# Optimization experiments

Hardware: AMD Instinct MI355X
Metric: run time of the kernel (lower is better)

Reference implementation:

```python
import jax, jax.numpy as jnp
import numpy as np

EPS = 216.0 / 24389.0
KAPPA = 24389.0 / 27.0
WP = jnp.array([0.95047, 1.0, 1.08883], dtype=jnp.float32)  # D65 white point
M_RGB2XYZ = jnp.array([[0.4124564, 0.3575761, 0.1804375],
                       [0.2126729, 0.7151522, 0.0721750],
                       [0.0193339, 0.1191920, 0.9503041]], dtype=jnp.float32)
M_XYZ2RGB = jnp.array([[3.2404542, -1.5371385, -0.4985314],
                       [-0.9692660, 1.8760108, 0.0415560],
                       [0.0556434, -0.2040259, 1.0572252]], dtype=jnp.float32)
GRID = 8          # cv2.createCLAHE tileGridSize=(8,8)
CLIP_LIMIT = 2.0  # cv2.createCLAHE clipLimit=2.0
NBINS = 256


def _srgb_to_linear(c):
    return jnp.where(c <= 0.04045, c / 12.92, ((c + 0.055) / 1.055) ** 2.4)


def _linear_to_srgb(c):
    c = jnp.maximum(c, 0.0)
    return jnp.where(c <= 0.0031308, c * 12.92, 1.055 * c ** (1.0 / 2.4) - 0.055)


def _rgb_to_lab(rgb):  # rgb [...,3] in [0,1]
    xyz = _srgb_to_linear(rgb) @ M_RGB2XYZ.T / WP
    f = jnp.where(xyz > EPS, jnp.cbrt(xyz), (KAPPA * xyz + 16.0) / 116.0)
    L = 116.0 * f[..., 1] - 16.0
    a = 500.0 * (f[..., 0] - f[..., 1])
    b = 200.0 * (f[..., 1] - f[..., 2])
    return L, a, b


def _lab_to_rgb(L, a, b):
    fy = (L + 16.0) / 116.0
    fx = fy + a / 500.0
    fz = fy - b / 200.0
    def finv(f):
        f3 = f ** 3
        return jnp.where(f3 > EPS, f3, (116.0 * f - 16.0) / KAPPA)
    xyz = jnp.stack([finv(fx), finv(fy), finv(fz)], axis=-1) * WP
    return jnp.clip(_linear_to_srgb(xyz @ M_XYZ2RGB.T), 0.0, 1.0)


def _quantize_L(L):  # cv2.normalize(..., 0, 255, NORM_MINMAX) per image + uint8 cast
    lmin = L.min(axis=(1, 2), keepdims=True)
    lmax = L.max(axis=(1, 2), keepdims=True)
    l255 = (L - lmin) / (lmax - lmin + 1e-6) * 255.0
    return jnp.clip(jnp.round(l255), 0, 255).astype(jnp.int32)


def _equalize_hist(l_int):  # cv2.equalizeHist per image, [N,H,W] int32 -> float levels
    N, H, W = l_int.shape
    seg = (jnp.arange(N, dtype=jnp.int32)[:, None, None] * NBINS + l_int).reshape(-1)
    hist = jax.ops.segment_sum(jnp.ones(seg.shape, jnp.float32), seg,
                               num_segments=N * NBINS).reshape(N, NBINS)
    lut = jnp.round(jnp.cumsum(hist, axis=1) * (255.0 / (H * W)))  # [N,256]
    return jnp.take_along_axis(lut, l_int.reshape(N, H * W), axis=1).reshape(N, H, W)


def _clahe(l_int):  # tiled clipped histogram equalization + bilinear LUT blend
    N, H, W = l_int.shape
    th, tw = H // GRID, W // GRID
    area = th * tw
    ty = jnp.arange(H, dtype=jnp.int32) // th
    tx = jnp.arange(W, dtype=jnp.int32) // tw
    tile = ty[:, None] * GRID + tx[None, :]                      # [H,W] tile id
    seg = ((jnp.arange(N, dtype=jnp.int32)[:, None, None] * (GRID * GRID) + tile)
           * NBINS + l_int).reshape(-1)
    hist = jax.ops.segment_sum(jnp.ones(seg.shape, jnp.float32), seg,
                               num_segments=N * GRID * GRID * NBINS
                               ).reshape(N, GRID, GRID, NBINS)
    limit = max(CLIP_LIMIT * area / NBINS, 1.0)                  # = 32 for 64x64 tiles
    clipped = jnp.minimum(hist, limit)
    excess = (hist - clipped).sum(axis=-1, keepdims=True)
    luts = jnp.round(jnp.cumsum(clipped + excess / NBINS, axis=-1) * (255.0 / area))
    # bilinear interpolation between the 4 neighbouring tile LUTs (border-clamped)
    cy = jnp.clip((jnp.arange(H, dtype=jnp.float32) + 0.5) / th - 0.5, 0.0, GRID - 1.0)
    cx = jnp.clip((jnp.arange(W, dtype=jnp.float32) + 0.5) / tw - 0.5, 0.0, GRID - 1.0)
    y0 = jnp.clip(jnp.floor(cy).astype(jnp.int32), 0, GRID - 2); y1 = y0 + 1
    x0 = jnp.clip(jnp.floor(cx).astype(jnp.int32), 0, GRID - 2); x1 = x0 + 1
    wy = (cy - y0)[:, None]
    wx = (cx - x0)[None, :]
    def per_image(lut, v):  # lut [GRID,GRID,256], v [H,W]
        v00 = lut[y0[:, None], x0[None, :], v]
        v01 = lut[y0[:, None], x1[None, :], v]
        v10 = lut[y1[:, None], x0[None, :], v]
        v11 = lut[y1[:, None], x1[None, :], v]
        top = v00 * (1.0 - wx) + v01 * wx
        bot = v10 * (1.0 - wx) + v11 * wx
        return top * (1.0 - wy) + bot * wy
    return jax.vmap(per_image)(luts, l_int)


def setup_inputs() -> dict:
    key = jax.random.key(0)
    x = jax.random.uniform(key, (16, 3, 512, 512), dtype=jnp.float32)
    return {"x": x}


def reference(x):
    rgb = jnp.transpose(x, (0, 2, 3, 1))          # NCHW -> NHWC
    L, a, b = _rgb_to_lab(rgb)
    l_int = _quantize_L(L)
    def recon(l255):
        out = _lab_to_rgb(l255 * (100.0 / 255.0), a, b)
        return jnp.transpose(out, (0, 3, 1, 2)) * 255.0  # uint8-valued like original
    return recon(_equalize_hist(l_int)), recon(_clahe(l_int))
```

## Files before the change

### kernel.cpp

```cpp
#include <hip/hip_runtime.h>

#define NIMG 16
#define HH 512
#define WW 512
#define HW (HH * WW)
#define NHW (NIMG * HW)
#define TILE 64
#define TILE_AREA (TILE * TILE)

#define EPSV ((float)(216.0 / 24389.0))
#define KAPV ((float)(24389.0 / 27.0))


__device__ __forceinline__ float pow24(float t) {
    float l   = __builtin_amdgcn_logf(t);
    float r   = __builtin_amdgcn_exp2f(l);
    float dl  = (t - r) * __builtin_amdgcn_rcpf(r) * 1.4426950408889634f;
    float ehi = 2.4f * l;
    float elo = __builtin_fmaf(2.4f, l, -ehi) + 2.4f * dl;
    float p   = __builtin_amdgcn_exp2f(ehi);
    return __builtin_fmaf(p * 0.6931471805599453f, elo, p);
}

__device__ __forceinline__ float cbrt_p(float v) {
    float l  = __builtin_amdgcn_logf(v);
    float t  = __builtin_amdgcn_exp2f(l * (1.0f / 3.0f));
    float t2 = t * t;
    float num = __builtin_fmaf(-t2, t, v);
    return __builtin_fmaf(num, __builtin_amdgcn_rcpf(3.0f * t2), t);
}

__device__ __forceinline__ float srgb2lin_p(float c) {
    float lin = c / 12.92f;
    float t   = (c + 0.055f) / 1.055f;
    return (c <= 0.04045f) ? lin : pow24(t);
}

__device__ __forceinline__ float fwd_p(float v) {
    return (v > EPSV) ? cbrt_p(v) : (KAPV * v + 16.0f) / 116.0f;
}

__device__ __forceinline__ float lin2srgb_f(float c) {
    c = fmaxf(c, 0.0f);
    float lo = c * 12.92f;
    float p  = __builtin_amdgcn_exp2f(__builtin_amdgcn_logf(c) * (float)(1.0 / 2.4));
    float hi = 1.055f * p - 0.055f;
    float r  = (c <= 0.0031308f) ? lo : hi;
    return fminf(fmaxf(r, 0.0f), 1.0f);
}

__device__ __forceinline__ float finv_f(float f) {
    float f3 = f * f * f;
    return (f3 > EPSV) ? f3 : (116.0f * f - 16.0f) * (float)(27.0 / 24389.0);
}

__device__ __forceinline__ void lab2rgb255_f(float L, float a, float b,
                                             float* R, float* G, float* B) {
    float fy = (L + 16.0f) * (float)(1.0 / 116.0);
    float fx = fy + a * (float)(1.0 / 500.0);
    float fz = fy - b * (float)(1.0 / 200.0);
    float X = finv_f(fx) * 0.95047f;
    float Y = finv_f(fy);
    float Z = finv_f(fz) * 1.08883f;
    *R = lin2srgb_f((float)3.2404542 * X + (float)-1.5371385 * Y + (float)-0.4985314 * Z) * 255.0f;
    *G = lin2srgb_f((float)-0.969266 * X + (float)1.8760108  * Y + (float)0.041556   * Z) * 255.0f;
    *B = lin2srgb_f((float)0.0556434 * X + (float)-0.2040259 * Y + (float)1.0572252  * Z) * 255.0f;
}

__device__ __forceinline__ unsigned f2o(float f) {
    unsigned b = __float_as_uint(f);
    return (b & 0x80000000u) ? ~b : (b | 0x80000000u);
}
__device__ __forceinline__ float o2f(unsigned o) {
    return __uint_as_float((o & 0x80000000u) ? (o ^ 0x80000000u) : ~o);
}


__global__ void k_init(unsigned* mm) {
    int t = blockIdx.x * 256 + threadIdx.x;
    if (t < NIMG * 64)
        mm[t] = ((t & 63) < 32) ? 0xFFFFFFFFu : 0u;
}

__global__ void k_lab(const float* __restrict__ x, float* __restrict__ Lbuf,
                      unsigned* __restrict__ mm) {
    int n = blockIdx.y;
    const float* img = x + (size_t)n * 3 * HW;
    float* Lp = Lbuf + (size_t)n * HW;
    int base = blockIdx.x * 2048;
    float mn = 1e30f, mx = -1e30f;
    for (int i = 0; i < 2; i++) {
        int p = base + i * 1024 + threadIdx.x * 4;
        float4 r4 = *(const float4*)(img + p);
        float4 g4 = *(const float4*)(img + HW + p);
        float4 b4 = *(const float4*)(img + 2 * HW + p);
        float4 L4;
        #pragma unroll
        for (int k = 0; k < 4; k++) {
            float rr = ((const float*)&r4)[k];
            float gg = ((const float*)&g4)[k];
            float bb = ((const float*)&b4)[k];
            float rl = srgb2lin_p(rr), gl = srgb2lin_p(gg), bl = srgb2lin_p(bb);
            float Y = ((float)0.2126729 * rl + (float)0.7151522 * gl + (float)0.072175  * bl);
            float L = 116.0f * fwd_p(Y) - 16.0f;
            ((float*)&L4)[k] = L;
            mn = fminf(mn, L);
            mx = fmaxf(mx, L);
        }
        *(float4*)(Lp + p) = L4;
    }
    for (int off = 32; off; off >>= 1) {
        mn = fminf(mn, __shfl_down(mn, off, 64));
        mx = fmaxf(mx, __shfl_down(mx, off, 64));
    }
    __shared__ float smn[4], smx[4];
    int wv = threadIdx.x >> 6, ln = threadIdx.x & 63;
    if (ln == 0) { smn[wv] = mn; smx[wv] = mx; }
    __syncthreads();
    if (threadIdx.x == 0) {
        mn = fminf(fminf(smn[0], smn[1]), fminf(smn[2], smn[3]));
        mx = fmaxf(fmaxf(smx[0], smx[1]), fmaxf(smx[2], smx[3]));
        atomicMin(&mm[n * 64], f2o(mn));
        atomicMax(&mm[n * 64 + 32], f2o(mx));
    }
}

__global__ void k_quant_hist(const float* __restrict__ Lbuf, const unsigned* __restrict__ mm,
                             unsigned char* __restrict__ li_arr, int* __restrict__ hist_tile,
                             float* __restrict__ lut_tile) {
    int n = blockIdx.y, tile = blockIdx.x;
    int ty = tile >> 3, tx = tile & 7;
    int t = threadIdx.x;
    __shared__ int sh[256];
    sh[t] = 0;
    __syncthreads();
    float lmin = o2f(mm[n * 64]), lmax = o2f(mm[n * 64 + 32]);
    float d = lmax - lmin + (float)1e-6;
    const float* Lp = Lbuf + (size_t)n * HW;
    unsigned char* lio = li_arr + (size_t)n * HW;
    for (int i = t; i < TILE_AREA; i += 256) {
        int r = i >> 6, c = i & 63;
        int p = (ty * TILE + r) * WW + tx * TILE + c;
        float l255 = (Lp[p] - lmin) / d * 255.0f;
        int li = (int)rintf(l255);
        li = min(max(li, 0), 255);
        lio[p] = (unsigned char)li;
        atomicAdd(&sh[li], 1);
    }
    __syncthreads();
    int h = sh[t];
    hist_tile[(n * 64 + tile) * 256 + t] = h;

    int cl = min(h, 32);
    int sum = cl;
    for (int off = 32; off; off >>= 1) sum += __shfl_down(sum, off, 64);
    __shared__ int wsum[4];
    if ((t & 63) == 0) wsum[t >> 6] = sum;
    __syncthreads();
    int total = wsum[0] + wsum[1] + wsum[2] + wsum[3];
    int exc = TILE_AREA - total;
    sh[t] = 256 * cl + exc;
    __syncthreads();
    for (int off = 1; off < 256; off <<= 1) {
        int v = sh[t];
        int add = (t >= off) ? sh[t - off] : 0;
        __syncthreads();
        sh[t] = v + add;
        __syncthreads();
    }
    lut_tile[(n * 64 + tile) * 256 + t] =
        rintf((float)sh[t] * (float)(255.0 / 1048576.0));
}

__global__ void k_eq_lut(const int* __restrict__ hist_tile, float* __restrict__ lut_eq) {
    int n = blockIdx.x, t = threadIdx.x;
    const int* ht = hist_tile + n * 64 * 256;
    int h = 0;
    for (int tile = 0; tile < 64; tile++) h += ht[tile * 256 + t];
    __shared__ int s[256];
    s[t] = h;
    __syncthreads();
    for (int off = 1; off < 256; off <<= 1) {
        int v = s[t];
        int add = (t >= off) ? s[t - off] : 0;
        __syncthreads();
        s[t] = v + add;
        __syncthreads();
    }
    lut_eq[n * 256 + t] = rintf((float)s[t] * (float)(255.0 / (double)HW));
}

__global__ void k_recon(const float* __restrict__ x, const unsigned char* __restrict__ li_arr,
                        const float* __restrict__ lut_eq, const float* __restrict__ lut_tile,
                        float* __restrict__ out) {
    int n = blockIdx.y, tile = blockIdx.x;
    int ty = tile >> 3, tx = tile & 7;
    int t = threadIdx.x;
    __shared__ float slut[9 * 256];
    __shared__ float seq[256];
    seq[t] = lut_eq[n * 256 + t];
    const float* lt = lut_tile + n * 64 * 256;
    for (int j = t; j < 9 * 256; j += 256) {
        int q = j >> 8;
        int jy = q / 3, jx = q % 3;
        int gy = min(max(ty - 1 + jy, 0), 7);
        int gx = min(max(tx - 1 + jx, 0), 7);
        slut[j] = lt[(gy * 8 + gx) * 256 + (j & 255)];
    }
    __syncthreads();

    const float* img = x + (size_t)n * 3 * HW;
    const unsigned char* lip = li_arr + (size_t)n * HW;
    float* o0 = out + (size_t)n * 3 * HW;
    float* o1 = out + (size_t)3 * NHW + (size_t)n * 3 * HW;

    for (int it = 0; it < 4; it++) {
        int j = it * 1024 + t * 4;
        int r = j >> 6, c = j & 63;
        int y = ty * TILE + r;
        int xb = tx * TILE + c;
        int p = y * WW + xb;

        float4 r4 = *(const float4*)(img + p);
        float4 g4 = *(const float4*)(img + HW + p);
        float4 b4 = *(const float4*)(img + 2 * HW + p);
        uchar4 li4 = *(const uchar4*)(lip + p);

        float cyf = fminf(fmaxf(((float)y + 0.5f) / 64.0f - 0.5f, 0.0f), 7.0f);
        int y0 = min((int)cyf, 6);
        float wy = cyf - (float)y0;
        int ly = y0 - ty + 1;

        float4 R0, G0, B0, R1, G1, B1;
        #pragma unroll
        for (int k = 0; k < 4; k++) {
            float rr = ((const float*)&r4)[k];
            float gg = ((const float*)&g4)[k];
            float bb = ((const float*)&b4)[k];
            float rl = srgb2lin_p(rr), gl = srgb2lin_p(gg), bl = srgb2lin_p(bb);
            float X = ((float)0.4124564 * rl + (float)0.3575761 * gl + (float)0.1804375 * bl) / (float)0.95047;
            float Y = ((float)0.2126729 * rl + (float)0.7151522 * gl + (float)0.072175  * bl);
            float Z = ((float)0.0193339 * rl + (float)0.119192  * gl + (float)0.9503041 * bl) / (float)1.08883;
            float fx = fwd_p(X), fy = fwd_p(Y), fz = fwd_p(Z);
            float A  = 500.0f * (fx - fy);
            float B2 = 200.0f * (fy - fz);

            int li = ((const unsigned char*)&li4)[k];
            float l_eq = seq[li];

            int xc = xb + k;
            float cxf = fminf(fmaxf(((float)xc + 0.5f) / 64.0f - 0.5f, 0.0f), 7.0f);
            int x0 = min((int)cxf, 6);
            float wx = cxf - (float)x0;
            int lx = x0 - tx + 1;
            int base = ((ly * 3 + lx) << 8) + li;
            float v00 = slut[base];
            float v01 = slut[base + 256];
            float v10 = slut[base + 768];
            float v11 = slut[base + 1024];
            float top = v00 * (1.0f - wx) + v01 * wx;
            float bot = v10 * (1.0f - wx) + v11 * wx;
            float l_cl = top * (1.0f - wy) + bot * wy;

            float R, G, B;
            lab2rgb255_f(l_eq * (float)(100.0 / 255.0), A, B2, &R, &G, &B);
            ((float*)&R0)[k] = R; ((float*)&G0)[k] = G; ((float*)&B0)[k] = B;
            lab2rgb255_f(l_cl * (float)(100.0 / 255.0), A, B2, &R, &G, &B);
            ((float*)&R1)[k] = R; ((float*)&G1)[k] = G; ((float*)&B1)[k] = B;
        }
        *(float4*)(o0 + p)          = R0;
        *(float4*)(o0 + HW + p)     = G0;
        *(float4*)(o0 + 2 * HW + p) = B0;
        *(float4*)(o1 + p)          = R1;
        *(float4*)(o1 + HW + p)     = G1;
        *(float4*)(o1 + 2 * HW + p) = B1;
    }
}

extern "C" void kernel_launch(void* const* d_in, const int* in_sizes, int n_in,
                              void* d_out, int out_size, void* d_ws, size_t ws_size,
                              hipStream_t stream) {
    const float* x = (const float*)d_in[0];
    float* out = (float*)d_out;
    char* ws = (char*)d_ws;

    float* Lbuf = (float*)ws;
    size_t off = (size_t)NHW * 4;
    unsigned char* li = (unsigned char*)(ws + off); off += NHW;
    int* hist_tile = (int*)(ws + off);    off += NIMG * 64 * 256 * 4;
    float* lut_eq = (float*)(ws + off);   off += NIMG * 256 * 4;
    float* lut_tile = (float*)(ws + off); off += NIMG * 64 * 256 * 4;
    unsigned* mm = (unsigned*)(ws + off); off += NIMG * 64 * 4;

    k_init<<<4, 256, 0, stream>>>(mm);
    k_lab<<<dim3(HW / 2048, NIMG), 256, 0, stream>>>(x, Lbuf, mm);
    k_quant_hist<<<dim3(64, NIMG), 256, 0, stream>>>(Lbuf, mm, li, hist_tile, lut_tile);
    k_eq_lut<<<NIMG, 256, 0, stream>>>(hist_tile, lut_eq);
    k_recon<<<dim3(64, NIMG), 256, 0, stream>>>(x, li, lut_eq, lut_tile, out);
}
```

Before: 185.7 us.

## Compute full Lab once, stash a/b in output buffer, merge kernels into three

The first kernel now computes the full Lab conversion per 64x64 tile and writes the a and b channels into the first output's G/B planes as scratch. The reconstruction kernel reads them back instead of reloading RGB and recomputing the forward transform. The global atomic min/max and init kernel are replaced by per-tile partials that the quant kernel reduces, and the equalization LUT scan is folded into the reconstruction kernel. This avoids recomputing the transcendental-heavy forward path and cuts two launches. In exchange it adds extra writes and reads of a/b, redundant histogram summation in every reconstruction block, and in-place reuse of the output buffer.

```diff
diff --git a/kernel.cpp b/kernel.cpp
--- a/kernel.cpp
+++ b/kernel.cpp
@@ -67,171 +67,27 @@
     *B = lin2srgb_f((float)0.0556434 * X + (float)-0.2040259 * Y + (float)1.0572252  * Z) * 255.0f;
 }
 
-__device__ __forceinline__ unsigned f2o(float f) {
-    unsigned b = __float_as_uint(f);
-    return (b & 0x80000000u) ? ~b : (b | 0x80000000u);
-}
-__device__ __forceinline__ float o2f(unsigned o) {
-    return __uint_as_float((o & 0x80000000u) ? (o ^ 0x80000000u) : ~o);
-}
-
-
-__global__ void k_init(unsigned* mm) {
-    int t = blockIdx.x * 256 + threadIdx.x;
-    if (t < NIMG * 64)
-        mm[t] = ((t & 63) < 32) ? 0xFFFFFFFFu : 0u;
-}
-
-__global__ void k_lab(const float* __restrict__ x, float* __restrict__ Lbuf,
-                      unsigned* __restrict__ mm) {
-    int n = blockIdx.y;
+__global__ void k1_lab(const float* __restrict__ x, float* __restrict__ Lbuf,
+                       float* __restrict__ out, float* __restrict__ tmn,
+                       float* __restrict__ tmx) {
+    int n = blockIdx.y, tile = blockIdx.x;
+    int b = (n << 6) + tile;
+    int ty = tile >> 3, tx = tile & 7;
+    int t = threadIdx.x;
     const float* img = x + (size_t)n * 3 * HW;
     float* Lp = Lbuf + (size_t)n * HW;
-    int base = blockIdx.x * 2048;
+    float* o0 = out + (size_t)n * 3 * HW;
+
     float mn = 1e30f, mx = -1e30f;
-    for (int i = 0; i < 2; i++) {
-        int p = base + i * 1024 + threadIdx.x * 4;
+    #pragma unroll
+    for (int it = 0; it < 4; it++) {
+        int j = it * 1024 + t * 4;
+        int r = j >> 6, c = j & 63;
+        int p = (ty * TILE + r) * WW + tx * TILE + c;
         float4 r4 = *(const float4*)(img + p);
         float4 g4 = *(const float4*)(img + HW + p);
         float4 b4 = *(const float4*)(img + 2 * HW + p);
-        float4 L4;
-        #pragma unroll
-        for (int k = 0; k < 4; k++) {
-            float rr = ((const float*)&r4)[k];
-            float gg = ((const float*)&g4)[k];
-            float bb = ((const float*)&b4)[k];
-            float rl = srgb2lin_p(rr), gl = srgb2lin_p(gg), bl = srgb2lin_p(bb);
-            float Y = ((float)0.2126729 * rl + (float)0.7151522 * gl + (float)0.072175  * bl);
-            float L = 116.0f * fwd_p(Y) - 16.0f;
-            ((float*)&L4)[k] = L;
-            mn = fminf(mn, L);
-            mx = fmaxf(mx, L);
-        }
-        *(float4*)(Lp + p) = L4;
-    }
-    for (int off = 32; off; off >>= 1) {
-        mn = fminf(mn, __shfl_down(mn, off, 64));
-        mx = fmaxf(mx, __shfl_down(mx, off, 64));
-    }
-    __shared__ float smn[4], smx[4];
-    int wv = threadIdx.x >> 6, ln = threadIdx.x & 63;
-    if (ln == 0) { smn[wv] = mn; smx[wv] = mx; }
-    __syncthreads();
-    if (threadIdx.x == 0) {
-        mn = fminf(fminf(smn[0], smn[1]), fminf(smn[2], smn[3]));
-        mx = fmaxf(fmaxf(smx[0], smx[1]), fmaxf(smx[2], smx[3]));
-        atomicMin(&mm[n * 64], f2o(mn));
-        atomicMax(&mm[n * 64 + 32], f2o(mx));
-    }
-}
-
-__global__ void k_quant_hist(const float* __restrict__ Lbuf, const unsigned* __restrict__ mm,
-                             unsigned char* __restrict__ li_arr, int* __restrict__ hist_tile,
-                             float* __restrict__ lut_tile) {
-    int n = blockIdx.y, tile = blockIdx.x;
-    int ty = tile >> 3, tx = tile & 7;
-    int t = threadIdx.x;
-    __shared__ int sh[256];
-    sh[t] = 0;
-    __syncthreads();
-    float lmin = o2f(mm[n * 64]), lmax = o2f(mm[n * 64 + 32]);
-    float d = lmax - lmin + (float)1e-6;
-    const float* Lp = Lbuf + (size_t)n * HW;
-    unsigned char* lio = li_arr + (size_t)n * HW;
-    for (int i = t; i < TILE_AREA; i += 256) {
-        int r = i >> 6, c = i & 63;
-        int p = (ty * TILE + r) * WW + tx * TILE + c;
-        float l255 = (Lp[p] - lmin) / d * 255.0f;
-        int li = (int)rintf(l255);
-        li = min(max(li, 0), 255);
-        lio[p] = (unsigned char)li;
-        atomicAdd(&sh[li], 1);
-    }
-    __syncthreads();
-    int h = sh[t];
-    hist_tile[(n * 64 + tile) * 256 + t] = h;
-
-    int cl = min(h, 32);
-    int sum = cl;
-    for (int off = 32; off; off >>= 1) sum += __shfl_down(sum, off, 64);
-    __shared__ int wsum[4];
-    if ((t & 63) == 0) wsum[t >> 6] = sum;
-    __syncthreads();
-    int total = wsum[0] + wsum[1] + wsum[2] + wsum[3];
-    int exc = TILE_AREA - total;
-    sh[t] = 256 * cl + exc;
-    __syncthreads();
-    for (int off = 1; off < 256; off <<= 1) {
-        int v = sh[t];
-        int add = (t >= off) ? sh[t - off] : 0;
-        __syncthreads();
-        sh[t] = v + add;
-        __syncthreads();
-    }
-    lut_tile[(n * 64 + tile) * 256 + t] =
-        rintf((float)sh[t] * (float)(255.0 / 1048576.0));
-}
-
-__global__ void k_eq_lut(const int* __restrict__ hist_tile, float* __restrict__ lut_eq) {
-    int n = blockIdx.x, t = threadIdx.x;
-    const int* ht = hist_tile + n * 64 * 256;
-    int h = 0;
-    for (int tile = 0; tile < 64; tile++) h += ht[tile * 256 + t];
-    __shared__ int s[256];
-    s[t] = h;
-    __syncthreads();
-    for (int off = 1; off < 256; off <<= 1) {
-        int v = s[t];
-        int add = (t >= off) ? s[t - off] : 0;
-        __syncthreads();
-        s[t] = v + add;
-        __syncthreads();
-    }
-    lut_eq[n * 256 + t] = rintf((float)s[t] * (float)(255.0 / (double)HW));
-}
-
-__global__ void k_recon(const float* __restrict__ x, const unsigned char* __restrict__ li_arr,
-                        const float* __restrict__ lut_eq, const float* __restrict__ lut_tile,
-                        float* __restrict__ out) {
-    int n = blockIdx.y, tile = blockIdx.x;
-    int ty = tile >> 3, tx = tile & 7;
-    int t = threadIdx.x;
-    __shared__ float slut[9 * 256];
-    __shared__ float seq[256];
-    seq[t] = lut_eq[n * 256 + t];
-    const float* lt = lut_tile + n * 64 * 256;
-    for (int j = t; j < 9 * 256; j += 256) {
-        int q = j >> 8;
-        int jy = q / 3, jx = q % 3;
-        int gy = min(max(ty - 1 + jy, 0), 7);
-        int gx = min(max(tx - 1 + jx, 0), 7);
-        slut[j] = lt[(gy * 8 + gx) * 256 + (j & 255)];
-    }
-    __syncthreads();
-
-    const float* img = x + (size_t)n * 3 * HW;
-    const unsigned char* lip = li_arr + (size_t)n * HW;
-    float* o0 = out + (size_t)n * 3 * HW;
-    float* o1 = out + (size_t)3 * NHW + (size_t)n * 3 * HW;
-
-    for (int it = 0; it < 4; it++) {
-        int j = it * 1024 + t * 4;
-        int r = j >> 6, c = j & 63;
-        int y = ty * TILE + r;
-        int xb = tx * TILE + c;
-        int p = y * WW + xb;
-
-        float4 r4 = *(const float4*)(img + p);
-        float4 g4 = *(const float4*)(img + HW + p);
-        float4 b4 = *(const float4*)(img + 2 * HW + p);
-        uchar4 li4 = *(const uchar4*)(lip + p);
-
-        float cyf = fminf(fmaxf(((float)y + 0.5f) / 64.0f - 0.5f, 0.0f), 7.0f);
-        int y0 = min((int)cyf, 6);
-        float wy = cyf - (float)y0;
-        int ly = y0 - ty + 1;
-
-        float4 R0, G0, B0, R1, G1, B1;
+        float4 L4, A4, B4;
         #pragma unroll
         for (int k = 0; k < 4; k++) {
             float rr = ((const float*)&r4)[k];
@@ -242,10 +98,163 @@
             float Y = ((float)0.2126729 * rl + (float)0.7151522 * gl + (float)0.072175  * bl);
             float Z = ((float)0.0193339 * rl + (float)0.119192  * gl + (float)0.9503041 * bl) / (float)1.08883;
             float fx = fwd_p(X), fy = fwd_p(Y), fz = fwd_p(Z);
-            float A  = 500.0f * (fx - fy);
-            float B2 = 200.0f * (fy - fz);
-
+            float L = 116.0f * fy - 16.0f;
+            ((float*)&L4)[k] = L;
+            ((float*)&A4)[k] = 500.0f * (fx - fy);
+            ((float*)&B4)[k] = 200.0f * (fy - fz);
+            mn = fminf(mn, L);
+            mx = fmaxf(mx, L);
+        }
+        *(float4*)(Lp + p)          = L4;
+        *(float4*)(o0 + HW + p)     = A4;
+        *(float4*)(o0 + 2 * HW + p) = B4;
+    }
+    for (int off = 32; off; off >>= 1) {
+        mn = fminf(mn, __shfl_down(mn, off, 64));
+        mx = fmaxf(mx, __shfl_down(mx, off, 64));
+    }
+    __shared__ float smn[4], smx[4];
+    int wv = t >> 6, ln = t & 63;
+    if (ln == 0) { smn[wv] = mn; smx[wv] = mx; }
+    __syncthreads();
+    if (t == 0) {
+        tmn[b] = fminf(fminf(smn[0], smn[1]), fminf(smn[2], smn[3]));
+        tmx[b] = fmaxf(fmaxf(smx[0], smx[1]), fmaxf(smx[2], smx[3]));
+    }
+}
+
+__global__ void k2_quant(const float* __restrict__ Lbuf, const float* __restrict__ tmn,
+                         const float* __restrict__ tmx, unsigned char* __restrict__ li_arr,
+                         int* __restrict__ hist_tile, float* __restrict__ lut_tile) {
+    int n = blockIdx.y, tile = blockIdx.x;
+    int b = (n << 6) + tile;
+    int ty = tile >> 3, tx = tile & 7;
+    int t = threadIdx.x;
+
+    __shared__ int sh[256];
+    __shared__ float sred2[2];
+    __shared__ int wsum[4];
+
+    if (t < 64) {
+        float v = tmn[(n << 6) + t];
+        for (int off = 32; off; off >>= 1) v = fminf(v, __shfl_down(v, off, 64));
+        if (t == 0) sred2[0] = v;
+    } else if (t < 128) {
+        float v = tmx[(n << 6) + (t - 64)];
+        for (int off = 32; off; off >>= 1) v = fmaxf(v, __shfl_down(v, off, 64));
+        if (t == 64) sred2[1] = v;
+    }
+    sh[t] = 0;
+    __syncthreads();
+    float lmin = sred2[0], lmax = sred2[1];
+    float d = lmax - lmin + (float)1e-6;
+
+    const float* Lp = Lbuf + (size_t)n * HW;
+    unsigned char* lio = li_arr + (size_t)n * HW;
+    #pragma unroll
+    for (int it = 0; it < 4; it++) {
+        int j = it * 1024 + t * 4;
+        int r = j >> 6, c = j & 63;
+        int p = (ty * TILE + r) * WW + tx * TILE + c;
+        float4 L4 = *(const float4*)(Lp + p);
+        uchar4 li4;
+        #pragma unroll
+        for (int k = 0; k < 4; k++) {
+            float l255 = (((const float*)&L4)[k] - lmin) / d * 255.0f;
+            int li = (int)rintf(l255);
+            li = min(max(li, 0), 255);
+            ((unsigned char*)&li4)[k] = (unsigned char)li;
+            atomicAdd(&sh[li], 1);
+        }
+        *(uchar4*)(lio + p) = li4;
+    }
+    __syncthreads();
+    int h = sh[t];
+    hist_tile[b * 256 + t] = h;
+
+    int cl = min(h, 32);
+    int sum = cl;
+    for (int off = 32; off; off >>= 1) sum += __shfl_down(sum, off, 64);
+    int wv = t >> 6, ln = t & 63;
+    if (ln == 0) wsum[wv] = sum;
+    __syncthreads();
+    int total = wsum[0] + wsum[1] + wsum[2] + wsum[3];
+    int exc = TILE_AREA - total;
+    sh[t] = 256 * cl + exc;
+    __syncthreads();
+    for (int off = 1; off < 256; off <<= 1) {
+        int v = sh[t];
+        int add = (t >= off) ? sh[t - off] : 0;
+        __syncthreads();
+        sh[t] = v + add;
+        __syncthreads();
+    }
+    lut_tile[b * 256 + t] = rintf((float)sh[t] * (float)(255.0 / 1048576.0));
+}
+
+__global__ void k3_recon(const unsigned char* __restrict__ li_arr,
+                         const int* __restrict__ hist_tile,
+                         const float* __restrict__ lut_tile,
+                         float* out) {
+    int n = blockIdx.y, tile = blockIdx.x;
+    int ty = tile >> 3, tx = tile & 7;
+    int t = threadIdx.x;
+
+    __shared__ int   sscan[256];
+    __shared__ float seq[256];
+    __shared__ float slut[9 * 256];
+
+    const int* ht = hist_tile + n * 64 * 256;
+    int h2 = 0;
+    for (int tile2 = 0; tile2 < 64; tile2++) h2 += ht[tile2 * 256 + t];
+    sscan[t] = h2;
+    __syncthreads();
+    for (int off = 1; off < 256; off <<= 1) {
+        int v = sscan[t];
+        int add = (t >= off) ? sscan[t - off] : 0;
+        __syncthreads();
+        sscan[t] = v + add;
+        __syncthreads();
+    }
+    seq[t] = rintf((float)sscan[t] * (float)(255.0 / (double)HW));
+
+    const float* lt = lut_tile + n * 64 * 256;
+    for (int j = t; j < 9 * 256; j += 256) {
+        int q = j >> 8;
+        int jy = q / 3, jx = q % 3;
+        int gy = min(max(ty - 1 + jy, 0), 7);
+        int gx = min(max(tx - 1 + jx, 0), 7);
+        slut[j] = lt[(gy * 8 + gx) * 256 + (j & 255)];
+    }
+    __syncthreads();
+
+    const unsigned char* lip = li_arr + (size_t)n * HW;
+    float* o0 = out + (size_t)n * 3 * HW;
+    float* o1 = out + (size_t)3 * NHW + (size_t)n * 3 * HW;
+
+    #pragma unroll
+    for (int it = 0; it < 4; it++) {
+        int j = it * 1024 + t * 4;
+        int r = j >> 6, c = j & 63;
+        int y = ty * TILE + r;
+        int xb = tx * TILE + c;
+        int p = y * WW + xb;
+
+        uchar4 li4 = *(const uchar4*)(lip + p);
+        float4 a4 = *(const float4*)(o0 + HW + p);
+        float4 b4 = *(const float4*)(o0 + 2 * HW + p);
+
+        float cyf = fminf(fmaxf(((float)y + 0.5f) / 64.0f - 0.5f, 0.0f), 7.0f);
+        int y0 = min((int)cyf, 6);
+        float wy = cyf - (float)y0;
+        int ly = y0 - ty + 1;
+
+        float4 R0, G0, B0, R1, G1, B1;
+        #pragma unroll
+        for (int k = 0; k < 4; k++) {
             int li = ((const unsigned char*)&li4)[k];
+            float A  = ((const float*)&a4)[k];
+            float B2 = ((const float*)&b4)[k];
             float l_eq = seq[li];
 
             int xc = xb + k;
@@ -287,14 +296,13 @@
     float* Lbuf = (float*)ws;
     size_t off = (size_t)NHW * 4;
     unsigned char* li = (unsigned char*)(ws + off); off += NHW;
-    int* hist_tile = (int*)(ws + off);    off += NIMG * 64 * 256 * 4;
-    float* lut_eq = (float*)(ws + off);   off += NIMG * 256 * 4;
-    float* lut_tile = (float*)(ws + off); off += NIMG * 64 * 256 * 4;
-    unsigned* mm = (unsigned*)(ws + off); off += NIMG * 64 * 4;
-
-    k_init<<<4, 256, 0, stream>>>(mm);
-    k_lab<<<dim3(HW / 2048, NIMG), 256, 0, stream>>>(x, Lbuf, mm);
-    k_quant_hist<<<dim3(64, NIMG), 256, 0, stream>>>(Lbuf, mm, li, hist_tile, lut_tile);
-    k_eq_lut<<<NIMG, 256, 0, stream>>>(hist_tile, lut_eq);
-    k_recon<<<dim3(64, NIMG), 256, 0, stream>>>(x, li, lut_eq, lut_tile, out);
-}
+    int* hist_tile = (int*)(ws + off);    off += (size_t)NIMG * 64 * 256 * 4;
+    float* lut_tile = (float*)(ws + off); off += (size_t)NIMG * 64 * 256 * 4;
+    float* tmn = (float*)(ws + off);      off += 1024 * 4;
+    float* tmx = (float*)(ws + off);      off += 1024 * 4;
+
+    dim3 grid(64, NIMG);
+    k1_lab<<<grid, 256, 0, stream>>>(x, Lbuf, out, tmn, tmx);
+    k2_quant<<<grid, 256, 0, stream>>>(Lbuf, tmn, tmx, li, hist_tile, lut_tile);
+    k3_recon<<<grid, 256, 0, stream>>>(li, hist_tile, lut_tile, out);
+}
```

Result: faster. 171.2 us (-7.8%).
